# Kernel optimization log

Measured on AMD Instinct MI355X. Metric: run time of the kernel, lower is better.

Reference implementation:

```python
import jax, jax.numpy as jnp
import numpy as np

B, C, H, W = 2, 512, 32, 32
HEADS = 8      # attention heads
GROUPS = 8     # offset groups (defaults to heads)
DH = 64        # dim_head
DF = 4         # downsample_factor
OFF_SCALE = 4.0
EPS = 1e-5


def _bn(t, gamma, beta):
    # eval-mode BatchNorm2d with running_mean=0, running_var=1
    s = gamma / jnp.sqrt(1.0 + EPS)
    return t * s[None, :, None, None] + beta[None, :, None, None]


def _gconv1x1(t, w):
    # grouped 1x1 conv (bias-free); w: (GROUPS, out_per_group, in_per_group)
    b, c, h, ww = t.shape
    o = jnp.einsum('bgci,goc->bgoi', t.reshape(b, GROUPS, c // GROUPS, h * ww), w)
    return o.reshape(b, GROUPS * w.shape[1], h, ww)


def _grid_sample(img, grid):
    # F.grid_sample: bilinear, padding_mode='zeros', align_corners=False
    # img: (N,Ci,Hi,Wi); grid: (N,Hg,Wg,2), grid[...,0]=x, grid[...,1]=y in [-1,1]
    N, Ci, Hi, Wi = img.shape
    gx = (grid[..., 0] + 1.0) * (Wi / 2.0) - 0.5
    gy = (grid[..., 1] + 1.0) * (Hi / 2.0) - 0.5
    x0 = jnp.floor(gx)
    y0 = jnp.floor(gy)
    wx = gx - x0
    wy = gy - y0

    def gather(im, ix, iy):
        valid = (ix >= 0) & (ix < Wi) & (iy >= 0) & (iy < Hi)
        ixc = jnp.clip(ix, 0, Wi - 1).astype(jnp.int32)
        iyc = jnp.clip(iy, 0, Hi - 1).astype(jnp.int32)
        return im[:, iyc, ixc] * valid[None].astype(im.dtype)

    def sample_one(im, x0, y0, wx, wy):
        v00 = gather(im, x0, y0)
        v01 = gather(im, x0 + 1, y0)
        v10 = gather(im, x0, y0 + 1)
        v11 = gather(im, x0 + 1, y0 + 1)
        wx = wx[None]
        wy = wy[None]
        return (v00 * (1 - wx) * (1 - wy) + v01 * wx * (1 - wy)
                + v10 * (1 - wx) * wy + v11 * wx * wy)

    return jax.vmap(sample_one)(img, x0, y0, wx, wy)


def _forward(x, bn1_g, bn1_b, bn2_g, bn2_b, qw, kw, vw, out_w, out_b,
             off_dw_w, off_dw_b, off_pw_w,
             cpb_w1, cpb_b1, cpb_w2, cpb_b2, cpb_w3, cpb_b3,
             mlp_w1, mlp_b1, mlp_w2, mlp_b2):
    b = x.shape[0]
    xn = _bn(x, bn1_g, bn1_b)
    # ---- deformable attention ----
    q = _gconv1x1(xn, qw)                                   # (b, 512, H, W)
    qg = q.reshape(b * GROUPS, DH, H, W)
    # to_offsets: depthwise conv k=6, s=4, p=1 -> GELU -> 1x1(64->2) -> tanh * offset_scale
    off = jax.lax.conv_general_dilated(
        qg, off_dw_w, (DF, DF), ((1, 1), (1, 1)),
        dimension_numbers=('NCHW', 'OIHW', 'NCHW'), feature_group_count=DH)
    off = jax.nn.gelu(off + off_dw_b[None, :, None, None], approximate=False)
    off = jnp.tanh(jnp.einsum('bchw,oc->bohw', off, off_pw_w)) * OFF_SCALE   # (b*G, 2, Hd, Wd)
    Hd, Wd = off.shape[-2], off.shape[-1]
    gy, gx = jnp.meshgrid(jnp.arange(Hd, dtype=x.dtype), jnp.arange(Wd, dtype=x.dtype), indexing='ij')
    vx = gx[None] + off[:, 0]
    vy = gy[None] + off[:, 1]
    # normalize_grid (lucidrains): first comp by (Hd-1), second by (Wd-1)
    nx = 2.0 * vx / max(Hd - 1, 1) - 1.0
    ny = 2.0 * vy / max(Wd - 1, 1) - 1.0
    vgrid_scaled = jnp.stack((nx, ny), axis=-1)             # (b*G, Hd, Wd, 2)
    kv = _grid_sample(xn.reshape(b * GROUPS, DH, H, W), vgrid_scaled)
    kv = kv.reshape(b, GROUPS * DH, Hd, Wd)
    k = _gconv1x1(kv, kw)
    v = _gconv1x1(kv, vw)
    scale = DH ** -0.5
    qh = q.reshape(b, HEADS, DH, H * W).transpose(0, 1, 3, 2) * scale    # (b,h,i,d)
    kh = k.reshape(b, HEADS, DH, Hd * Wd).transpose(0, 1, 3, 2)          # (b,h,j,d)
    vh = v.reshape(b, HEADS, DH, Hd * Wd).transpose(0, 1, 3, 2)
    # continuous relative position bias (CPB)
    qgy, qgx = jnp.meshgrid(jnp.arange(H, dtype=x.dtype), jnp.arange(W, dtype=x.dtype), indexing='ij')
    grid_q = jnp.stack((2.0 * qgx / max(H - 1, 1) - 1.0,
                        2.0 * qgy / max(W - 1, 1) - 1.0), axis=-1).reshape(1, H * W, 2)
    grid_kv = vgrid_scaled.reshape(b * GROUPS, Hd * Wd, 2)
    pos = grid_q[:, :, None, :] - grid_kv[:, None, :, :]    # (b*G, i, j, 2)
    bias = jnp.sign(pos) * jnp.log1p(jnp.abs(pos))
    bias = jax.nn.relu(bias @ cpb_w1 + cpb_b1)
    bias = jax.nn.relu(bias @ cpb_w2 + cpb_b2)
    bias = (bias @ cpb_w3 + cpb_b3).reshape(b, GROUPS, H * W, Hd * Wd)   # heads//groups == 1
    sim = jnp.einsum('bhid,bhjd->bhij', qh, kh) + bias
    attn = jax.nn.softmax(sim, axis=-1)
    out = jnp.einsum('bhij,bhjd->bhid', attn, vh)
    out = out.transpose(0, 1, 3, 2).reshape(b, HEADS * DH, H, W)
    out = jnp.einsum('bchw,oc->bohw', out, out_w) + out_b[None, :, None, None]
    x = x + out
    # ---- conv1x1 MLP ----
    xn2 = _bn(x, bn2_g, bn2_b)
    h1 = jax.nn.gelu(jnp.einsum('bchw,oc->bohw', xn2, mlp_w1) + mlp_b1[None, :, None, None],
                     approximate=False)
    return x + jnp.einsum('bchw,oc->bohw', h1, mlp_w2) + mlp_b2[None, :, None, None]


def setup_inputs():
    ks = jax.random.split(jax.random.key(0), 16)
    w = lambda k, shape: jax.random.normal(k, shape, dtype=jnp.float32) * 0.02
    return {
        'x': jax.random.normal(ks[0], (B, C, H, W), dtype=jnp.float32),
        'bn1_g': jnp.ones((C,), jnp.float32),
        'bn1_b': jnp.zeros((C,), jnp.float32),
        'bn2_g': jnp.ones((C,), jnp.float32),
        'bn2_b': jnp.zeros((C,), jnp.float32),
        'qw': w(ks[1], (GROUPS, DH, C // GROUPS)),
        'kw': w(ks[2], (GROUPS, DH, C // GROUPS)),
        'vw': w(ks[3], (GROUPS, DH, C // GROUPS)),
        'out_w': w(ks[4], (C, HEADS * DH)),
        'out_b': jnp.zeros((C,), jnp.float32),
        'off_dw_w': w(ks[5], (DH, 1, 6, 6)),
        'off_dw_b': jnp.zeros((DH,), jnp.float32),
        'off_pw_w': w(ks[6], (2, DH)),
        'cpb_w1': w(ks[7], (2, 128)),
        'cpb_b1': jnp.zeros((128,), jnp.float32),
        'cpb_w2': w(ks[8], (128, 128)),
        'cpb_b2': jnp.zeros((128,), jnp.float32),
        'cpb_w3': w(ks[9], (128, 1)),
        'cpb_b3': jnp.zeros((1,), jnp.float32),
        'mlp_w1': w(ks[10], (4 * C, C)),
        'mlp_b1': jnp.zeros((4 * C,), jnp.float32),
        'mlp_w2': w(ks[11], (C, 4 * C)),
        'mlp_b2': jnp.zeros((C,), jnp.float32),
    }


def reference(x, bn1_g, bn1_b, bn2_g, bn2_b, qw, kw, vw, out_w, out_b,
              off_dw_w, off_dw_b, off_pw_w,
              cpb_w1, cpb_b1, cpb_w2, cpb_b2, cpb_w3, cpb_b3,
              mlp_w1, mlp_b1, mlp_w2, mlp_b2):
    return _forward(x, bn1_g, bn1_b, bn2_g, bn2_b, qw, kw, vw, out_w, out_b,
                    off_dw_w, off_dw_b, off_pw_w,
                    cpb_w1, cpb_b1, cpb_w2, cpb_b2, cpb_w3, cpb_b3,
                    mlp_w1, mlp_b1, mlp_w2, mlp_b2)
```

## Files before the change

kernel.cpp:

```cpp
#include <hip/hip_runtime.h>
#include <hip/hip_bf16.h>
#include <math.h>

#define BB 2
#define CC 512
#define HH 32
#define WW 32
#define HWP 1024
#define GG 8
#define DH 64
#define HD 8
#define WD 8
#define JJ 64
#define BG 16
#define EPS 1e-5f

typedef __attribute__((ext_vector_type(8))) short short8;
typedef __attribute__((ext_vector_type(4))) short s16x4;
typedef __attribute__((ext_vector_type(4))) float f32x4;
typedef __attribute__((ext_vector_type(4))) unsigned short u16x4;
typedef __attribute__((ext_vector_type(4))) unsigned int u32x4;

static __device__ __forceinline__ short f2bf(float x) {
    unsigned u = __builtin_bit_cast(unsigned, x);
    u += 0x7FFFu + ((u >> 16) & 1u);
    return (short)(u >> 16);
}

__global__ void k_wpack(const float* __restrict__ qw, const float* __restrict__ ow,
                        const float* __restrict__ w1, const float* __restrict__ w2,
                        unsigned short* __restrict__ wp) {
    int idx = blockIdx.x * 256 + threadIdx.x;
    float v;
    if (idx < 32768) v = qw[idx];
    else if (idx < 294912) v = ow[idx - 32768];
    else if (idx < 1343488) v = w1[idx - 294912];
    else v = w2[idx - 1343488];
    wp[idx] = (unsigned short)f2bf(v);
}

__global__ __launch_bounds__(256) void k_qgemm(
    const float* __restrict__ x, const float* __restrict__ g1,
    const float* __restrict__ b1, const unsigned short* __restrict__ qwp,
    float* __restrict__ q) {
    __shared__ __align__(16) short As[64][72];
    __shared__ __align__(16) short Bs[64][72];
    int blk = blockIdx.x;
    int bg = blk >> 4, nt = blk & 15;
    int b = bg >> 3, g = bg & 7;
    int i0 = nt * 64;
    int tid = threadIdx.x, lane = tid & 63, wv = tid >> 6;
    int wm = (wv >> 1) * 32, wn = (wv & 1) * 32;
    int l15 = lane & 15, quad = lane >> 4;
    const float invs = 1.0f / sqrtf(1.0f + EPS);
    {
        int c4 = (tid & 15) * 4;
        int ob = tid >> 4;
#pragma unroll
        for (int p = 0; p < 4; p++) {
            int o = ob + p * 16;
            u16x4 v = *(const u16x4*)(qwp + (size_t)(g * 64 + o) * 64 + c4);
            *(u16x4*)&As[o][c4] = v;
        }
    }
    {
        int i4 = (tid & 15) * 4;
        int cb = tid >> 4;
#pragma unroll
        for (int p = 0; p < 4; p++) {
            int c = cb + p * 16;
            f32x4 v = *(const f32x4*)(x + (size_t)(b * CC + g * 64 + c) * HWP + i0 + i4);
            float sc = g1[g * 64 + c] * invs;
            float sh = b1[g * 64 + c];
            Bs[i4 + 0][c] = f2bf(fmaf(v.x, sc, sh));
            Bs[i4 + 1][c] = f2bf(fmaf(v.y, sc, sh));
            Bs[i4 + 2][c] = f2bf(fmaf(v.z, sc, sh));
            Bs[i4 + 3][c] = f2bf(fmaf(v.w, sc, sh));
        }
    }
    __syncthreads();
    f32x4 acc[2][2];
#pragma unroll
    for (int a = 0; a < 2; a++)
#pragma unroll
        for (int c = 0; c < 2; c++) acc[a][c] = (f32x4){0.f, 0.f, 0.f, 0.f};
#pragma unroll
    for (int ks = 0; ks < 2; ks++) {
        short8 af0 = *(const short8*)&As[wm + l15][ks * 32 + quad * 8];
        short8 af1 = *(const short8*)&As[wm + 16 + l15][ks * 32 + quad * 8];
        short8 bf0 = *(const short8*)&Bs[wn + l15][ks * 32 + quad * 8];
        short8 bf1 = *(const short8*)&Bs[wn + 16 + l15][ks * 32 + quad * 8];
        acc[0][0] = __builtin_amdgcn_mfma_f32_16x16x32_bf16(af0, bf0, acc[0][0], 0, 0, 0);
        acc[0][1] = __builtin_amdgcn_mfma_f32_16x16x32_bf16(af0, bf1, acc[0][1], 0, 0, 0);
        acc[1][0] = __builtin_amdgcn_mfma_f32_16x16x32_bf16(af1, bf0, acc[1][0], 0, 0, 0);
        acc[1][1] = __builtin_amdgcn_mfma_f32_16x16x32_bf16(af1, bf1, acc[1][1], 0, 0, 0);
    }
#pragma unroll
    for (int im = 0; im < 2; im++)
#pragma unroll
        for (int r = 0; r < 4; r++) {
            int m = wm + im * 16 + quad * 4 + r;
#pragma unroll
            for (int in_ = 0; in_ < 2; in_++) {
                int n = wn + in_ * 16 + l15;
                q[(size_t)(bg * 64 + m) * HWP + i0 + n] = acc[im][in_][r];
            }
        }
}

__global__ void k_off(const float* __restrict__ q, const float* __restrict__ dww,
                      const float* __restrict__ dwb, const float* __restrict__ pw,
                      float* __restrict__ vgrid) {
    int blk = blockIdx.x;
    int bg = blk >> 6;
    int hd = (blk >> 3) & 7;
    int wd = blk & 7;
    int ch = threadIdx.x;
    const float* qch = q + (size_t)(bg * 64 + ch) * HWP;
    float acc = 0.f;
#pragma unroll
    for (int kh = 0; kh < 6; kh++) {
        int hin = hd * 4 - 1 + kh;
        if (hin < 0 || hin >= HH) continue;
#pragma unroll
        for (int kw_ = 0; kw_ < 6; kw_++) {
            int win = wd * 4 - 1 + kw_;
            if (win < 0 || win >= WW) continue;
            acc = fmaf(qch[hin * WW + win], dww[ch * 36 + kh * 6 + kw_], acc);
        }
    }
    acc += dwb[ch];
    float ge = 0.5f * acc * (1.0f + erff(acc * 0.7071067811865475f));
    float p0 = ge * pw[ch];
    float p1 = ge * pw[64 + ch];
#pragma unroll
    for (int off = 32; off; off >>= 1) {
        p0 += __shfl_xor(p0, off);
        p1 += __shfl_xor(p1, off);
    }
    if (ch == 0) {
        float off0 = tanhf(p0) * 4.0f;
        float off1 = tanhf(p1) * 4.0f;
        float vx = (float)wd + off0;
        float vy = (float)hd + off1;
        float nx = 2.0f * vx / 7.0f - 1.0f;
        float ny = 2.0f * vy / 7.0f - 1.0f;
        vgrid[blk * 2] = nx;
        vgrid[blk * 2 + 1] = ny;
    }
}

__global__ __launch_bounds__(64) void k_skv(
    const float* __restrict__ x, const float* __restrict__ g1,
    const float* __restrict__ b1, const float* __restrict__ vgrid,
    const float* __restrict__ kw, const float* __restrict__ vw,
    float* __restrict__ kk, float* __restrict__ vv) {
    __shared__ float sm[64];
    int blk = blockIdx.x;
    int bg = blk >> 6, j = blk & 63;
    int g = bg & 7, b = bg >> 3;
    int t = threadIdx.x;
    const float invs = 1.0f / sqrtf(1.0f + EPS);
    {
        int cg = g * 64 + t;
        float s = g1[cg] * invs;
        float bv = b1[cg];
        float nx = vgrid[blk * 2];
        float ny = vgrid[blk * 2 + 1];
        float gx = (nx + 1.0f) * 16.0f - 0.5f;
        float gy = (ny + 1.0f) * 16.0f - 0.5f;
        float x0f = floorf(gx), y0f = floorf(gy);
        float wx = gx - x0f, wy = gy - y0f;
        int x0 = (int)x0f, y0 = (int)y0f;
        const float* im = x + (size_t)(b * CC + cg) * HWP;
        float sx = 0.f, sw = 0.f;
        float w00 = (1 - wx) * (1 - wy), w01 = wx * (1 - wy);
        float w10 = (1 - wx) * wy, w11 = wx * wy;
        if (x0 >= 0 && x0 < WW && y0 >= 0 && y0 < HH)                 { sx += w00 * im[y0 * WW + x0];           sw += w00; }
        if (x0 + 1 >= 0 && x0 + 1 < WW && y0 >= 0 && y0 < HH)         { sx += w01 * im[y0 * WW + x0 + 1];       sw += w01; }
        if (x0 >= 0 && x0 < WW && y0 + 1 >= 0 && y0 + 1 < HH)         { sx += w10 * im[(y0 + 1) * WW + x0];     sw += w10; }
        if (x0 + 1 >= 0 && x0 + 1 < WW && y0 + 1 >= 0 && y0 + 1 < HH) { sx += w11 * im[(y0 + 1) * WW + x0 + 1]; sw += w11; }
        sm[t] = s * sx + bv * sw;
    }
    __syncthreads();
    const float* kwr = kw + (size_t)(g * 64 + t) * 64;
    const float* vwr = vw + (size_t)(g * 64 + t) * 64;
    float ak = 0.f, av = 0.f;
#pragma unroll
    for (int c = 0; c < 64; c++) {
        float tv = sm[c];
        ak = fmaf(tv, kwr[c], ak);
        av = fmaf(tv, vwr[c], av);
    }
    kk[(size_t)bg * 4096 + j * 64 + t] = ak;
    vv[(size_t)bg * 4096 + j * 64 + t] = av;
}

__global__ void k_w2pack(const float* __restrict__ w2, unsigned short* __restrict__ w2p) {
    int idx = blockIdx.x * 256 + threadIdx.x;
    int k = idx >> 7, n = idx & 127;
    int dest = ((((n >> 4) * 4 + (k >> 5)) * 64) + (((k >> 3) & 3) * 16) + (n & 15)) * 8 + (k & 7);
    w2p[dest] = (unsigned short)f2bf(w2[idx]);
}

__global__ __launch_bounds__(256) void k_cpb(
    const float* __restrict__ vgrid, const unsigned short* __restrict__ w2p,
    const float* __restrict__ w1, const float* __restrict__ b1,
    const float* __restrict__ b2, const float* __restrict__ w3,
    const float* __restrict__ b3, float* __restrict__ bias) {
    __shared__ __align__(16) short w2fs[16384];
    __shared__ __align__(16) float coef[640];
    int tid = threadIdx.x;
    {
        const u32x4* src = (const u32x4*)w2p;
        u32x4* dst = (u32x4*)w2fs;
        for (int c = tid; c < 2048; c += 256) dst[c] = src[c];
    }
    if (tid < 256) coef[tid] = w1[tid];
    else if (tid < 384) coef[tid] = b1[tid - 256];
    else if (tid < 512) coef[tid] = b2[tid - 384];
    if (tid >= 128 && tid < 256) coef[512 + tid - 128] = w3[tid - 128];
    float bias3 = b3[0];
    __syncthreads();

    int lane = tid & 63;
    int wv = tid >> 6;
    int l15 = lane & 15;
    int quad = lane >> 4;

#pragma unroll 1
    for (int it = 0; it < 4; it++) {
        int p = (blockIdx.x * 4 + it) * 4 + wv;
        int bg = p >> 11;
        int i = (p >> 1) & 1023;
        int jbase = (p & 1) * 32;
        int hi = i >> 5, wi = i & 31;
        float qx = 2.0f * (float)wi / 31.0f - 1.0f;
        float qy = 2.0f * (float)hi / 31.0f - 1.0f;

        int jA = jbase + l15;
        float gkxA = vgrid[(bg * 64 + jA) * 2];
        float gkyA = vgrid[(bg * 64 + jA) * 2 + 1];
        float gkxB = vgrid[(bg * 64 + jA + 16) * 2];
        float gkyB = vgrid[(bg * 64 + jA + 16) * 2 + 1];
        float p0 = qx - gkxA, p1 = qy - gkyA;
        float s0a = copysignf(log1pf(fabsf(p0)), p0);
        float s1a = copysignf(log1pf(fabsf(p1)), p1);
        p0 = qx - gkxB; p1 = qy - gkyB;
        float s0b = copysignf(log1pf(fabsf(p0)), p0);
        float s1b = copysignf(log1pf(fabsf(p1)), p1);

        short8 hA[4], hB[4];
#pragma unroll
        for (int kc = 0; kc < 4; kc++) {
            f32x4 cu0 = *(const f32x4*)&coef[kc * 32 + quad * 8];
            f32x4 cu1 = *(const f32x4*)&coef[kc * 32 + quad * 8 + 4];
            f32x4 cv0 = *(const f32x4*)&coef[128 + kc * 32 + quad * 8];
            f32x4 cv1 = *(const f32x4*)&coef[128 + kc * 32 + quad * 8 + 4];
            f32x4 cb0 = *(const f32x4*)&coef[256 + kc * 32 + quad * 8];
            f32x4 cb1 = *(const f32x4*)&coef[256 + kc * 32 + quad * 8 + 4];
            u32x4 pa, pb;
#pragma unroll
            for (int j2 = 0; j2 < 4; j2++) {
                int e0 = 2 * j2, e1 = 2 * j2 + 1;
                float u0 = (e0 < 4) ? cu0[e0] : cu1[e0 - 4];
                float u1 = (e1 < 4) ? cu0[e1] : cu1[e1 - 4];
                float v0 = (e0 < 4) ? cv0[e0] : cv1[e0 - 4];
                float v1 = (e1 < 4) ? cv0[e1] : cv1[e1 - 4];
                float c0 = (e0 < 4) ? cb0[e0] : cb1[e0 - 4];
                float c1 = (e1 < 4) ? cb0[e1] : cb1[e1 - 4];
                unsigned a0 = __builtin_bit_cast(unsigned,
                    fmaxf(fmaf(s0a, u0, fmaf(s1a, v0, c0)), 0.f)) + 0x8000u;
                unsigned a1 = __builtin_bit_cast(unsigned,
                    fmaxf(fmaf(s0a, u1, fmaf(s1a, v1, c1)), 0.f)) + 0x8000u;
                pa[j2] = __builtin_amdgcn_perm(a1, a0, 0x07060302);
                unsigned b0 = __builtin_bit_cast(unsigned,
                    fmaxf(fmaf(s0b, u0, fmaf(s1b, v0, c0)), 0.f)) + 0x8000u;
                unsigned b1_ = __builtin_bit_cast(unsigned,
                    fmaxf(fmaf(s0b, u1, fmaf(s1b, v1, c1)), 0.f)) + 0x8000u;
                pb[j2] = __builtin_amdgcn_perm(b1_, b0, 0x07060302);
            }
            hA[kc] = __builtin_bit_cast(short8, pa);
            hB[kc] = __builtin_bit_cast(short8, pb);
        }

        float psumA = 0.f, psumB = 0.f;
#pragma unroll 1
        for (int nt = 0; nt < 8; nt++) {
            f32x4 accA = (f32x4){0.f, 0.f, 0.f, 0.f};
            f32x4 accB = (f32x4){0.f, 0.f, 0.f, 0.f};
#pragma unroll
            for (int kc = 0; kc < 4; kc++) {
                short8 af = *(const short8*)(w2fs + (((nt * 4 + kc) * 64) + lane) * 8);
                accA = __builtin_amdgcn_mfma_f32_16x16x32_bf16(af, hA[kc], accA, 0, 0, 0);
                accB = __builtin_amdgcn_mfma_f32_16x16x32_bf16(af, hB[kc], accB, 0, 0, 0);
            }
            f32x4 b2q = *(const f32x4*)&coef[384 + nt * 16 + quad * 4];
            f32x4 w3q = *(const f32x4*)&coef[512 + nt * 16 + quad * 4];
#pragma unroll
            for (int r = 0; r < 4; r++) {
                psumA = fmaf(fmaxf(accA[r] + b2q[r], 0.f), w3q[r], psumA);
                psumB = fmaf(fmaxf(accB[r] + b2q[r], 0.f), w3q[r], psumB);
            }
        }
        psumA += __shfl_xor(psumA, 16);
        psumA += __shfl_xor(psumA, 32);
        psumB += __shfl_xor(psumB, 16);
        psumB += __shfl_xor(psumB, 32);
        if (quad == 0) {
            bias[(size_t)(p * 2 + 0) * 16 + l15] = psumA + bias3;
            bias[(size_t)(p * 2 + 1) * 16 + l15] = psumB + bias3;
        }
    }
}

__global__ __launch_bounds__(256) void k_attn(
    const float* __restrict__ q, const float* __restrict__ kk,
    const float* __restrict__ vv, const float* __restrict__ bias,
    unsigned short* __restrict__ ao) {
    __shared__ __align__(16) short Ks[64][72];
    __shared__ __align__(16) short Vt[64][72];
    __shared__ __align__(16) short Qs[64][72];
    __shared__ __align__(16) short Ps[4][16][72];
    int blk = blockIdx.x;
    int bg = blk >> 4;
    int chunk = blk & 15;
    int i0 = chunk * 64;
    int b = bg >> 3, g = bg & 7;
    int tid = threadIdx.x, lane = tid & 63, wv = tid >> 6;
    int l15 = lane & 15, quad = lane >> 4;

    const float* kbase = kk + (size_t)bg * 4096;
    const float* vbase = vv + (size_t)bg * 4096;
#pragma unroll
    for (int it = 0; it < 4; it++) {
        int e4 = it * 1024 + tid * 4;
        int j = e4 >> 6, d = e4 & 63;
        f32x4 k4 = *(const f32x4*)(kbase + e4);
        s16x4 s = {f2bf(k4.x), f2bf(k4.y), f2bf(k4.z), f2bf(k4.w)};
        *(s16x4*)&Ks[j][d] = s;
        f32x4 v4 = *(const f32x4*)(vbase + e4);
        Vt[d + 0][j] = f2bf(v4.x);
        Vt[d + 1][j] = f2bf(v4.y);
        Vt[d + 2][j] = f2bf(v4.z);
        Vt[d + 3][j] = f2bf(v4.w);
    }
    const float* qbase = q + (size_t)(b * CC + g * 64) * HWP + i0;
#pragma unroll
    for (int it = 0; it < 4; it++) {
        int e4 = it * 1024 + tid * 4;
        int d = e4 >> 6, i = e4 & 63;
        f32x4 q4 = *(const f32x4*)(qbase + (size_t)d * HWP + i);
        Qs[i + 0][d] = f2bf(q4.x * 0.125f);
        Qs[i + 1][d] = f2bf(q4.y * 0.125f);
        Qs[i + 2][d] = f2bf(q4.z * 0.125f);
        Qs[i + 3][d] = f2bf(q4.w * 0.125f);
    }
    __syncthreads();

    int iw = wv * 16;
    f32x4 Sacc[4];
#pragma unroll
    for (int nt = 0; nt < 4; nt++) Sacc[nt] = (f32x4){0.f, 0.f, 0.f, 0.f};
#pragma unroll
    for (int ks = 0; ks < 2; ks++) {
        short8 aq = *(const short8*)&Qs[iw + l15][quad * 8 + ks * 32];
#pragma unroll
        for (int nt = 0; nt < 4; nt++) {
            short8 bk = *(const short8*)&Ks[nt * 16 + l15][quad * 8 + ks * 32];
            Sacc[nt] = __builtin_amdgcn_mfma_f32_16x16x32_bf16(aq, bk, Sacc[nt], 0, 0, 0);
        }
    }
    const float* bp = bias + ((size_t)bg * 1024 + i0 + iw + quad * 4) * 64 + l15;
    float Sv[4][4];
#pragma unroll
    for (int nt = 0; nt < 4; nt++)
#pragma unroll
        for (int r = 0; r < 4; r++)
            Sv[nt][r] = Sacc[nt][r] + bp[r * 64 + nt * 16];
#pragma unroll
    for (int r = 0; r < 4; r++) {
        float m = fmaxf(fmaxf(Sv[0][r], Sv[1][r]), fmaxf(Sv[2][r], Sv[3][r]));
        m = fmaxf(m, __shfl_xor(m, 1));
        m = fmaxf(m, __shfl_xor(m, 2));
        m = fmaxf(m, __shfl_xor(m, 4));
        m = fmaxf(m, __shfl_xor(m, 8));
        float l = 0.f;
#pragma unroll
        for (int nt = 0; nt < 4; nt++) { Sv[nt][r] = expf(Sv[nt][r] - m); l += Sv[nt][r]; }
        l += __shfl_xor(l, 1);
        l += __shfl_xor(l, 2);
        l += __shfl_xor(l, 4);
        l += __shfl_xor(l, 8);
        float inv = 1.0f / l;
#pragma unroll
        for (int nt = 0; nt < 4; nt++)
            Ps[wv][quad * 4 + r][nt * 16 + l15] = f2bf(Sv[nt][r] * inv);
    }
    f32x4 Oacc[4];
#pragma unroll
    for (int nt = 0; nt < 4; nt++) Oacc[nt] = (f32x4){0.f, 0.f, 0.f, 0.f};
#pragma unroll
    for (int ks = 0; ks < 2; ks++) {
        short8 ap = *(const short8*)&Ps[wv][l15][quad * 8 + ks * 32];
#pragma unroll
        for (int nt = 0; nt < 4; nt++) {
            short8 bv = *(const short8*)&Vt[nt * 16 + l15][quad * 8 + ks * 32];
            Oacc[nt] = __builtin_amdgcn_mfma_f32_16x16x32_bf16(ap, bv, Oacc[nt], 0, 0, 0);
        }
    }
    __syncthreads();
#pragma unroll
    for (int nt = 0; nt < 4; nt++) {
        s16x4 o4 = {f2bf(Oacc[nt][0]), f2bf(Oacc[nt][1]), f2bf(Oacc[nt][2]), f2bf(Oacc[nt][3])};
        *(s16x4*)&Qs[nt * 16 + l15][iw + quad * 4] = o4;
    }
    __syncthreads();
    {
        int d = tid >> 2;
        int ic = (tid & 3) * 16;
        short8 a = *(const short8*)&Qs[d][ic];
        short8 c = *(const short8*)&Qs[d][ic + 8];
        unsigned short* dst = ao + (size_t)(b * CC + g * 64 + d) * HWP + i0 + ic;
        *(short8*)dst = a;
        *(short8*)(dst + 8) = c;
    }
}

template<int EPI, int KD, int MT, bool BBF, bool BN>
__global__ __launch_bounds__(256) void k_gemm(
    const unsigned short* __restrict__ A, const void* __restrict__ Bp,
    const float* __restrict__ resid, const float* __restrict__ bias,
    void* __restrict__ outp,
    const float* __restrict__ bns, const float* __restrict__ bnb) {
    constexpr int MM = MT * 64;
    __shared__ __align__(16) short As[64][72];
    __shared__ __align__(16) short Bs[64][72];
    int tid = threadIdx.x;
    int blk = blockIdx.x;
    int mt = blk & (MT - 1);
    int nb = blk / MT;
    int bb = nb >> 4, nt = nb & 15;
    int m0 = mt * 64, i0 = nt * 64;
    int lane = tid & 63, wv = tid >> 6;
    int wm = (wv >> 1) * 32, wn = (wv & 1) * 32;
    int l15 = lane & 15, quad = lane >> 4;
    const unsigned short* Af = A + (size_t)m0 * KD;
    const float* Bf = (const float*)Bp;
    const unsigned short* Bh = (const unsigned short*)Bp;
    const float invs = 1.0f / sqrtf(1.0f + EPS);

    f32x4 acc[2][2];
#pragma unroll
    for (int a = 0; a < 2; a++)
#pragma unroll
        for (int c = 0; c < 2; c++) acc[a][c] = (f32x4){0.f, 0.f, 0.f, 0.f};

    for (int k0 = 0; k0 < KD; k0 += 64) {
        __syncthreads();
        {
            int kk4 = (tid & 15) * 4;
            int myb = tid >> 4;
#pragma unroll
            for (int p = 0; p < 4; p++) {
                int my = myb + p * 16;
                u16x4 v = *(const u16x4*)(Af + (size_t)my * KD + k0 + kk4);
                *(u16x4*)&As[my][kk4] = v;
            }
        }
        {
            int i4 = (tid & 15) * 4;
            int kyb = tid >> 4;
#pragma unroll
            for (int p = 0; p < 4; p++) {
                int ky = kyb + p * 16;
                size_t goff = (size_t)bb * KD * HWP + (size_t)(k0 + ky) * HWP + i0 + i4;
                if (BBF) {
                    u16x4 v = *(const u16x4*)(Bh + goff);
                    Bs[i4 + 0][ky] = (short)v.x;
                    Bs[i4 + 1][ky] = (short)v.y;
                    Bs[i4 + 2][ky] = (short)v.z;
                    Bs[i4 + 3][ky] = (short)v.w;
                } else {
                    f32x4 v = *(const f32x4*)(Bf + goff);
                    if (BN) {
                        float sc = bns[k0 + ky] * invs;
                        float sh = bnb[k0 + ky];
                        v.x = fmaf(v.x, sc, sh);
                        v.y = fmaf(v.y, sc, sh);
                        v.z = fmaf(v.z, sc, sh);
                        v.w = fmaf(v.w, sc, sh);
                    }
                    Bs[i4 + 0][ky] = f2bf(v.x);
                    Bs[i4 + 1][ky] = f2bf(v.y);
                    Bs[i4 + 2][ky] = f2bf(v.z);
                    Bs[i4 + 3][ky] = f2bf(v.w);
                }
            }
        }
        __syncthreads();
#pragma unroll
        for (int ks = 0; ks < 2; ks++) {
            short8 af0 = *(const short8*)&As[wm + l15][ks * 32 + quad * 8];
            short8 af1 = *(const short8*)&As[wm + 16 + l15][ks * 32 + quad * 8];
            short8 bf0 = *(const short8*)&Bs[wn + l15][ks * 32 + quad * 8];
            short8 bf1 = *(const short8*)&Bs[wn + 16 + l15][ks * 32 + quad * 8];
            acc[0][0] = __builtin_amdgcn_mfma_f32_16x16x32_bf16(af0, bf0, acc[0][0], 0, 0, 0);
            acc[0][1] = __builtin_amdgcn_mfma_f32_16x16x32_bf16(af0, bf1, acc[0][1], 0, 0, 0);
            acc[1][0] = __builtin_amdgcn_mfma_f32_16x16x32_bf16(af1, bf0, acc[1][0], 0, 0, 0);
            acc[1][1] = __builtin_amdgcn_mfma_f32_16x16x32_bf16(af1, bf1, acc[1][1], 0, 0, 0);
        }
    }

    float* outF = (float*)outp;
    unsigned short* outH = (unsigned short*)outp;
#pragma unroll
    for (int im = 0; im < 2; im++) {
#pragma unroll
        for (int r = 0; r < 4; r++) {
            int m = m0 + wm + im * 16 + quad * 4 + r;
            float bv = bias[m];
#pragma unroll
            for (int in_ = 0; in_ < 2; in_++) {
                int n = i0 + wn + in_ * 16 + l15;
                size_t idx = ((size_t)bb * MM + m) * HWP + n;
                float v = acc[im][in_][r] + bv;
                if constexpr (EPI == 1) {
                    float ge = 0.5f * v * (1.0f + erff(v * 0.7071067811865475f));
                    outH[idx] = (unsigned short)f2bf(ge);
                } else {
                    outF[idx] = v + resid[idx];
                }
            }
        }
    }
}

extern "C" void kernel_launch(void* const* d_in, const int* in_sizes, int n_in,
                              void* d_out, int out_size, void* d_ws, size_t ws_size,
                              hipStream_t stream) {
    const float* x      = (const float*)d_in[0];
    const float* bn1_g  = (const float*)d_in[1];
    const float* bn1_b  = (const float*)d_in[2];
    const float* bn2_g  = (const float*)d_in[3];
    const float* bn2_b  = (const float*)d_in[4];
    const float* qw     = (const float*)d_in[5];
    const float* kw     = (const float*)d_in[6];
    const float* vw     = (const float*)d_in[7];
    const float* out_w  = (const float*)d_in[8];
    const float* out_b  = (const float*)d_in[9];
    const float* off_dw_w = (const float*)d_in[10];
    const float* off_dw_b = (const float*)d_in[11];
    const float* off_pw_w = (const float*)d_in[12];
    const float* cpb_w1 = (const float*)d_in[13];
    const float* cpb_b1 = (const float*)d_in[14];
    const float* cpb_w2 = (const float*)d_in[15];
    const float* cpb_b2 = (const float*)d_in[16];
    const float* cpb_w3 = (const float*)d_in[17];
    const float* cpb_b3 = (const float*)d_in[18];
    const float* mlp_w1 = (const float*)d_in[19];
    const float* mlp_b1 = (const float*)d_in[20];
    const float* mlp_w2 = (const float*)d_in[21];
    const float* mlp_b2 = (const float*)d_in[22];

    float* ws = (float*)d_ws;
    float* q     = ws + 1048576;
    float* vgrid = ws + 2097152;
    float* kk    = ws + 2164736;
    float* vv    = ws + 2230272;
    unsigned short* w2p = (unsigned short*)(ws + 2295808);
    unsigned short* ao  = (unsigned short*)(ws + 2312192);
    float* xo    = ws + 3360768;
    float* h1of  = ws + 4409344;
    float* biasb = h1of;
    unsigned short* h1o = (unsigned short*)h1of;
    unsigned short* wp  = (unsigned short*)(ws + 6506496);
    unsigned short* qwp  = wp;
    unsigned short* owp  = wp + 32768;
    unsigned short* w1p  = wp + 294912;
    unsigned short* w2mp = wp + 1343488;

    hipLaunchKernelGGL(k_wpack, dim3(9344), dim3(256), 0, stream, qw, out_w, mlp_w1, mlp_w2, wp);
    hipLaunchKernelGGL(k_qgemm, dim3(256), dim3(256), 0, stream, x, bn1_g, bn1_b, qwp, q);
    hipLaunchKernelGGL(k_off, dim3(1024), dim3(64), 0, stream, q, off_dw_w, off_dw_b, off_pw_w, vgrid);
    hipLaunchKernelGGL(k_skv, dim3(1024), dim3(64), 0, stream, x, bn1_g, bn1_b, vgrid, kw, vw, kk, vv);
    hipLaunchKernelGGL(k_w2pack, dim3(64), dim3(256), 0, stream, cpb_w2, w2p);
    hipLaunchKernelGGL(k_cpb, dim3(2048), dim3(256), 0, stream,
                       vgrid, w2p, cpb_w1, cpb_b1, cpb_b2, cpb_w3, cpb_b3, biasb);
    hipLaunchKernelGGL(k_attn, dim3(256), dim3(256), 0, stream, q, kk, vv, biasb, ao);
    k_gemm<0, 512, 8, true, false><<<dim3(256), dim3(256), 0, stream>>>(
        owp, ao, x, out_b, xo, nullptr, nullptr);
    k_gemm<1, 512, 32, false, true><<<dim3(1024), dim3(256), 0, stream>>>(
        w1p, xo, nullptr, mlp_b1, h1o, bn2_g, bn2_b);
    k_gemm<2, 2048, 8, true, false><<<dim3(256), dim3(256), 0, stream>>>(
        w2mp, h1o, xo, mlp_b2, d_out, nullptr, nullptr);
}
```

Measured before the change: 284.5 us.

## Fuse BN2 into out-proj epilogue emitting bf16, merge cpb weight pack

The out-projection GEMM epilogue now applies the second BatchNorm and writes a bf16 copy of the normalized residual. The MLP first GEMM then reads bf16 input directly instead of loading fp32, applying BN and converting on every tile load. The cpb w2 packing kernel is folded into the main weight-pack kernel to save a launch, and the cpb inner loop is unrolled by 2. This costs an extra bf16 write in the out-proj GEMM but halves the B-operand traffic and removes the per-tile conversion work in the large MLP GEMM.

```diff
diff --git a/kernel.cpp b/kernel.cpp
--- a/kernel.cpp
+++ b/kernel.cpp
@@ -29,14 +29,22 @@
 
 __global__ void k_wpack(const float* __restrict__ qw, const float* __restrict__ ow,
                         const float* __restrict__ w1, const float* __restrict__ w2,
-                        unsigned short* __restrict__ wp) {
+                        const float* __restrict__ cw2, unsigned short* __restrict__ wp,
+                        unsigned short* __restrict__ w2p) {
     int idx = blockIdx.x * 256 + threadIdx.x;
-    float v;
-    if (idx < 32768) v = qw[idx];
-    else if (idx < 294912) v = ow[idx - 32768];
-    else if (idx < 1343488) v = w1[idx - 294912];
-    else v = w2[idx - 1343488];
-    wp[idx] = (unsigned short)f2bf(v);
+    if (idx < 2392064) {
+        float v;
+        if (idx < 32768) v = qw[idx];
+        else if (idx < 294912) v = ow[idx - 32768];
+        else if (idx < 1343488) v = w1[idx - 294912];
+        else v = w2[idx - 1343488];
+        wp[idx] = (unsigned short)f2bf(v);
+    } else if (idx < 2408448) {
+        int i2 = idx - 2392064;
+        int k = i2 >> 7, n = i2 & 127;
+        int dest = ((((n >> 4) * 4 + (k >> 5)) * 64) + (((k >> 3) & 3) * 16) + (n & 15)) * 8 + (k & 7);
+        w2p[dest] = (unsigned short)f2bf(cw2[i2]);
+    }
 }
 
 __global__ __launch_bounds__(256) void k_qgemm(
@@ -196,13 +204,6 @@
     vv[(size_t)bg * 4096 + j * 64 + t] = av;
 }
 
-__global__ void k_w2pack(const float* __restrict__ w2, unsigned short* __restrict__ w2p) {
-    int idx = blockIdx.x * 256 + threadIdx.x;
-    int k = idx >> 7, n = idx & 127;
-    int dest = ((((n >> 4) * 4 + (k >> 5)) * 64) + (((k >> 3) & 3) * 16) + (n & 15)) * 8 + (k & 7);
-    w2p[dest] = (unsigned short)f2bf(w2[idx]);
-}
-
 __global__ __launch_bounds__(256) void k_cpb(
     const float* __restrict__ vgrid, const unsigned short* __restrict__ w2p,
     const float* __restrict__ w1, const float* __restrict__ b1,
@@ -285,7 +286,7 @@
         }
 
         float psumA = 0.f, psumB = 0.f;
-#pragma unroll 1
+#pragma unroll 2
         for (int nt = 0; nt < 8; nt++) {
             f32x4 accA = (f32x4){0.f, 0.f, 0.f, 0.f};
             f32x4 accB = (f32x4){0.f, 0.f, 0.f, 0.f};
@@ -427,11 +428,11 @@
     }
 }
 
-template<int EPI, int KD, int MT, bool BBF, bool BN>
+template<int EPI, int KD, int MT, bool BBF>
 __global__ __launch_bounds__(256) void k_gemm(
     const unsigned short* __restrict__ A, const void* __restrict__ Bp,
     const float* __restrict__ resid, const float* __restrict__ bias,
-    void* __restrict__ outp,
+    void* __restrict__ outp, unsigned short* __restrict__ out2,
     const float* __restrict__ bns, const float* __restrict__ bnb) {
     constexpr int MM = MT * 64;
     __shared__ __align__(16) short As[64][72];
@@ -483,14 +484,6 @@
                     Bs[i4 + 3][ky] = (short)v.w;
                 } else {
                     f32x4 v = *(const f32x4*)(Bf + goff);
-                    if (BN) {
-                        float sc = bns[k0 + ky] * invs;
-                        float sh = bnb[k0 + ky];
-                        v.x = fmaf(v.x, sc, sh);
-                        v.y = fmaf(v.y, sc, sh);
-                        v.z = fmaf(v.z, sc, sh);
-                        v.w = fmaf(v.w, sc, sh);
-                    }
                     Bs[i4 + 0][ky] = f2bf(v.x);
                     Bs[i4 + 1][ky] = f2bf(v.y);
                     Bs[i4 + 2][ky] = f2bf(v.z);
@@ -528,6 +521,10 @@
                 if constexpr (EPI == 1) {
                     float ge = 0.5f * v * (1.0f + erff(v * 0.7071067811865475f));
                     outH[idx] = (unsigned short)f2bf(ge);
+                } else if constexpr (EPI == 3) {
+                    float vr = v + resid[idx];
+                    outF[idx] = vr;
+                    out2[idx] = (unsigned short)f2bf(fmaf(vr, bns[m] * invs, bnb[m]));
                 } else {
                     outF[idx] = v + resid[idx];
                 }
@@ -570,6 +567,7 @@
     float* vv    = ws + 2230272;
     unsigned short* w2p = (unsigned short*)(ws + 2295808);
     unsigned short* ao  = (unsigned short*)(ws + 2312192);
+    unsigned short* xn2 = (unsigned short*)(ws + 2836480);
     float* xo    = ws + 3360768;
     float* h1of  = ws + 4409344;
     float* biasb = h1of;
@@ -580,18 +578,18 @@
     unsigned short* w1p  = wp + 294912;
     unsigned short* w2mp = wp + 1343488;
 
-    hipLaunchKernelGGL(k_wpack, dim3(9344), dim3(256), 0, stream, qw, out_w, mlp_w1, mlp_w2, wp);
+    hipLaunchKernelGGL(k_wpack, dim3(9408), dim3(256), 0, stream,
+                       qw, out_w, mlp_w1, mlp_w2, cpb_w2, wp, w2p);
     hipLaunchKernelGGL(k_qgemm, dim3(256), dim3(256), 0, stream, x, bn1_g, bn1_b, qwp, q);
     hipLaunchKernelGGL(k_off, dim3(1024), dim3(64), 0, stream, q, off_dw_w, off_dw_b, off_pw_w, vgrid);
     hipLaunchKernelGGL(k_skv, dim3(1024), dim3(64), 0, stream, x, bn1_g, bn1_b, vgrid, kw, vw, kk, vv);
-    hipLaunchKernelGGL(k_w2pack, dim3(64), dim3(256), 0, stream, cpb_w2, w2p);
     hipLaunchKernelGGL(k_cpb, dim3(2048), dim3(256), 0, stream,
                        vgrid, w2p, cpb_w1, cpb_b1, cpb_b2, cpb_w3, cpb_b3, biasb);
     hipLaunchKernelGGL(k_attn, dim3(256), dim3(256), 0, stream, q, kk, vv, biasb, ao);
-    k_gemm<0, 512, 8, true, false><<<dim3(256), dim3(256), 0, stream>>>(
-        owp, ao, x, out_b, xo, nullptr, nullptr);
-    k_gemm<1, 512, 32, false, true><<<dim3(1024), dim3(256), 0, stream>>>(
-        w1p, xo, nullptr, mlp_b1, h1o, bn2_g, bn2_b);
-    k_gemm<2, 2048, 8, true, false><<<dim3(256), dim3(256), 0, stream>>>(
-        w2mp, h1o, xo, mlp_b2, d_out, nullptr, nullptr);
-}
+    k_gemm<3, 512, 8, true><<<dim3(256), dim3(256), 0, stream>>>(
+        owp, ao, x, out_b, xo, xn2, bn2_g, bn2_b);
+    k_gemm<1, 512, 32, true><<<dim3(1024), dim3(256), 0, stream>>>(
+        w1p, xn2, nullptr, mlp_b1, h1o, nullptr, nullptr, nullptr);
+    k_gemm<2, 2048, 8, true><<<dim3(256), dim3(256), 0, stream>>>(
+        w2mp, h1o, xo, mlp_b2, d_out, nullptr, nullptr, nullptr);
+}
```

Measured after the change: 276.1 us. -3.0%, faster.
